# Performance work log

Measured on AMD Instinct MI355X. Metric: run time of the kernel, lower is better.

The kernel has to match this reference:

```python
import jax, jax.numpy as jnp
import numpy as np

DIM = 768
HEADS = 12
FF = 3072
EPS = 1e-6


def setup_inputs() -> dict:
    key = jax.random.key(0)
    ks = jax.random.split(key, 12)
    B, S, D, F_ = 64, 197, DIM, FF
    s = 0.02
    inp = {
        "x": jax.random.normal(ks[0], (B, S, D), jnp.float32),
        "Wq": jax.random.normal(ks[1], (D, D), jnp.float32) * s,
        "bq": jnp.zeros((D,), jnp.float32),
        "Wk": jax.random.normal(ks[2], (D, D), jnp.float32) * s,
        "bk": jnp.zeros((D,), jnp.float32),
        "Wv": jax.random.normal(ks[3], (D, D), jnp.float32) * s,
        "bv": jnp.zeros((D,), jnp.float32),
        "Wo": jax.random.normal(ks[4], (D, D), jnp.float32) * s,
        "bo": jnp.zeros((D,), jnp.float32),
        "ln1_w": jnp.ones((D,), jnp.float32),
        "ln1_b": jnp.zeros((D,), jnp.float32),
        "W1": jax.random.normal(ks[5], (D, F_), jnp.float32) * s,
        "b1": jnp.zeros((F_,), jnp.float32),
        "W2": jax.random.normal(ks[6], (F_, D), jnp.float32) * s,
        "b2": jnp.zeros((D,), jnp.float32),
        "ln2_w": jnp.ones((D,), jnp.float32),
        "ln2_b": jnp.zeros((D,), jnp.float32),
        "mask": jnp.ones((B, S), jnp.int32),
    }
    return inp


def _layernorm(x, w, b):
    m = jnp.mean(x, axis=-1, keepdims=True)
    v = jnp.mean(jnp.square(x - m), axis=-1, keepdims=True)  # unbiased=False
    return (x - m) / jnp.sqrt(v + EPS) * w + b


def _block(x, mask_f, Wq, bq, Wk, bk, Wv, bv, Wo, bo, ln1_w, ln1_b, W1, b1, W2, b2, ln2_w, ln2_b):
    B, S, D = x.shape
    H = HEADS
    Dh = D // H
    # --- attention (pre-norm) ---
    h = _layernorm(x, ln1_w, ln1_b)
    q = (h @ Wq + bq).reshape(B, S, H, Dh).transpose(0, 2, 1, 3)
    k = (h @ Wk + bk).reshape(B, S, H, Dh).transpose(0, 2, 1, 3)
    v = (h @ Wv + bv).reshape(B, S, H, Dh).transpose(0, 2, 1, 3)
    scores = jnp.einsum("bhqd,bhkd->bhqk", q, k) / jnp.sqrt(jnp.float32(Dh))
    scores = scores - 10000.0 * (1.0 - mask_f[:, None, None, :])
    probs = jax.nn.softmax(scores, axis=-1)
    attn = jnp.einsum("bhqk,bhkd->bhqd", probs, v).transpose(0, 2, 1, 3).reshape(B, S, D)
    x = x + (attn @ Wo + bo)  # dropout = identity (eval)
    # --- FFN (pre-norm), exact erf GELU (F.gelu default) ---
    h = _layernorm(x, ln2_w, ln2_b)
    h = jax.nn.gelu(h @ W1 + b1, approximate=False)
    x = x + (h @ W2 + b2)
    return x


def reference(x, Wq, bq, Wk, bk, Wv, bv, Wo, bo, ln1_w, ln1_b, W1, b1, W2, b2, ln2_w, ln2_b, mask):
    mask_f = mask.astype(jnp.float32)
    return _block(x, mask_f, Wq, bq, Wk, bk, Wv, bv, Wo, bo, ln1_w, ln1_b, W1, b1, W2, b2, ln2_w, ln2_b)
```

## Files before the change

kernel.cpp:

```cpp
#include <hip/hip_runtime.h>
#include <stdint.h>

#define B_   64
#define S_   197
#define D_   768
#define H_   12
#define F_   3072
#define BS_  (B_ * S_)

typedef __attribute__((ext_vector_type(8))) short short8;
typedef __attribute__((ext_vector_type(4))) float f32x4;

__device__ __forceinline__ float bf2f(unsigned short h) {
    union { unsigned int u; float f; } v; v.u = ((unsigned int)h) << 16; return v.f;
}
__device__ __forceinline__ unsigned short f2bf(float f) {
    union { float f; unsigned int u; } v; v.f = f;
    unsigned int r = v.u + 0x7FFFu + ((v.u >> 16) & 1u);
    return (unsigned short)(r >> 16);
}

__device__ __forceinline__ void g2l16(const void* g, void* l) {
    __builtin_amdgcn_global_load_lds(
        (const __attribute__((address_space(1))) unsigned int*)g,
        (__attribute__((address_space(3))) unsigned int*)l, 16, 0, 0);
}

__device__ __forceinline__ float gelu_f(float c) {
    float z = fabsf(c) * 0.70710678118f;
    float t = __builtin_amdgcn_rcpf(1.f + 0.3275911f * z);
    float p = ((((1.061405429f * t - 1.453152027f) * t + 1.421413741f) * t
               - 0.284496736f) * t + 0.254829592f) * t;
    float erfv = 1.f - p * __expf(-z * z);
    erfv = c < 0.f ? -erfv : erfv;
    return 0.5f * c * (1.f + erfv);
}

__global__ __launch_bounds__(256)
void transpose_all(const float* __restrict__ Wq, const float* __restrict__ Wk,
                   const float* __restrict__ Wv, const float* __restrict__ Wo,
                   const float* __restrict__ W1, const float* __restrict__ W2,
                   const float* __restrict__ bq, const float* __restrict__ bk,
                   const float* __restrict__ bv,
                   unsigned short* __restrict__ wqkvT, unsigned short* __restrict__ woT,
                   unsigned short* __restrict__ w1T, unsigned short* __restrict__ w2T,
                   float* __restrict__ bcat) {
    int blk = blockIdx.x;
    int tx = threadIdx.x, ty = threadIdx.y;
    if (blk == 6912) {
        for (int i = ty * 32 + tx; i < 2304; i += 256)
            bcat[i] = i < 768 ? bq[i] : (i < 1536 ? bk[i - 768] : bv[i - 1536]);
        return;
    }
    const float* W; unsigned short* Wt; int K, N, rel, nx;
    if (blk < 2304) {
        int m = blk / 576; rel = blk - m * 576; K = 768; N = 768; nx = 24;
        W  = m == 0 ? Wq : m == 1 ? Wk : m == 2 ? Wv : Wo;
        Wt = m < 3 ? wqkvT + (size_t)m * 768 * 768 : woT;
    } else if (blk < 4608) {
        rel = blk - 2304; K = 768; N = 3072; nx = 96; W = W1; Wt = w1T;
    } else {
        rel = blk - 4608; K = 3072; N = 768; nx = 24; W = W2; Wt = w2T;
    }
    int n0 = (rel % nx) * 32, k0 = (rel / nx) * 32;
    __shared__ float t[32][33];
#pragma unroll
    for (int i = ty; i < 32; i += 8) t[i][tx] = W[(size_t)(k0 + i) * N + n0 + tx];
    __syncthreads();
#pragma unroll
    for (int i = ty; i < 32; i += 8) Wt[(size_t)(n0 + i) * K + k0 + tx] = f2bf(t[tx][i]);
}

__global__ __launch_bounds__(256)
void ln_kernel(const float* __restrict__ x, const float* __restrict__ w,
               const float* __restrict__ b, unsigned short* __restrict__ out) {
    int row = blockIdx.x; size_t base = (size_t)row * 768;
    int tid = threadIdx.x;
    float v0 = x[base + tid], v1 = x[base + tid + 256], v2 = x[base + tid + 512];
    float s1 = v0 + v1 + v2;
    float s2 = v0 * v0 + v1 * v1 + v2 * v2;
#pragma unroll
    for (int off = 32; off > 0; off >>= 1) { s1 += __shfl_xor(s1, off); s2 += __shfl_xor(s2, off); }
    __shared__ float sa[4], sb[4];
    int w4 = tid >> 6;
    if ((tid & 63) == 0) { sa[w4] = s1; sb[w4] = s2; }
    __syncthreads();
    s1 = sa[0] + sa[1] + sa[2] + sa[3];
    s2 = sb[0] + sb[1] + sb[2] + sb[3];
    float mean = s1 * (1.f / 768.f);
    float var  = s2 * (1.f / 768.f) - mean * mean;
    float rstd = rsqrtf(var + 1e-6f);
    out[base + tid]       = f2bf((v0 - mean) * rstd * w[tid]       + b[tid]);
    out[base + tid + 256] = f2bf((v1 - mean) * rstd * w[tid + 256] + b[tid + 256]);
    out[base + tid + 512] = f2bf((v2 - mean) * rstd * w[tid + 512] + b[tid + 512]);
}

template<int MODE>
__global__ __launch_bounds__(64, 3)
void gemm1w(const unsigned short* __restrict__ A, const unsigned short* __restrict__ Bt,
            const float* __restrict__ bias, const float* __restrict__ resid,
            void* __restrict__ out, int M, int N, int K, int NSUP) {
    constexpr int BK = 32;
    __shared__ unsigned short As[2][64 * BK];
    __shared__ unsigned short Bs[2][64 * BK];
    const int l = threadIdx.x;
    const int lr = l & 15, lg = l >> 4;

    const int nN = gridDim.x, nM = gridDim.y;
    const int nTot = nN * nM;
    const int orig = blockIdx.x + nN * blockIdx.y;
    const int q8 = nTot >> 3, r8 = nTot & 7;
    const int xcd = orig & 7, idx = orig >> 3;
    const int rank = (xcd < r8 ? xcd * (q8 + 1) : r8 * (q8 + 1) + (xcd - r8) * q8) + idx;
    const int fullg = nM * NSUP;
    const int sup = rank / fullg;
    const int rem = rank - sup * fullg;
    const int n0s = sup * NSUP;
    int wsup = nN - n0s; if (wsup > NSUP) wsup = NSUP;
    const int mloc = rem / wsup;
    const int nloc = rem - mloc * wsup;
    const int bm0 = mloc * 64;
    const int bn0 = (n0s + nloc) * 64;

    const int srow = l >> 2;
    const int slb  = (l & 3) ^ ((l >> 3) & 3);
    const unsigned short* aBase = A  + (size_t)(bm0 + srow) * K + slb * 8;
    const unsigned short* bBase = Bt + (size_t)(bn0 + srow) * K + slb * 8;
    auto stage = [&](int buf, int kt) {
        const int k0 = kt * BK;
#pragma unroll
        for (int c = 0; c < 4; ++c) {
            g2l16(aBase + (size_t)c * 16 * K + k0, &As[buf][c * 16 * BK]);
            g2l16(bBase + (size_t)c * 16 * K + k0, &Bs[buf][c * 16 * BK]);
        }
    };

    f32x4 acc[4][4];
#pragma unroll
    for (int i = 0; i < 4; ++i)
#pragma unroll
        for (int j = 0; j < 4; ++j) acc[i][j] = (f32x4){0.f, 0.f, 0.f, 0.f};

    const int NK = K / BK;
    stage(0, 0);
    stage(1, 1);

    const int rblk = (lg ^ ((lr >> 1) & 3)) * 8;
    for (int kt = 0; kt < NK; ++kt) {
        const int buf = kt & 1;
        if (kt + 1 < NK) { asm volatile("s_waitcnt vmcnt(8)" ::: "memory"); }
        else             { asm volatile("s_waitcnt vmcnt(0)" ::: "memory"); }
        __builtin_amdgcn_sched_barrier(0);
        short8 af[4], bfr[4];
#pragma unroll
        for (int mt = 0; mt < 4; ++mt) af[mt]  = *(const short8*)&As[buf][(mt * 16 + lr) * BK + rblk];
#pragma unroll
        for (int nt = 0; nt < 4; ++nt) bfr[nt] = *(const short8*)&Bs[buf][(nt * 16 + lr) * BK + rblk];
        __builtin_amdgcn_sched_barrier(0);
        if (kt + 2 < NK) stage(buf, kt + 2);
#pragma unroll
        for (int mt = 0; mt < 4; ++mt)
#pragma unroll
            for (int nt = 0; nt < 4; ++nt)
                acc[mt][nt] = __builtin_amdgcn_mfma_f32_16x16x32_bf16(af[mt], bfr[nt], acc[mt][nt], 0, 0, 0);
    }

#pragma unroll
    for (int mt = 0; mt < 4; ++mt)
#pragma unroll
        for (int nt = 0; nt < 4; ++nt)
#pragma unroll
            for (int r = 0; r < 4; ++r) {
                int gm = bm0 + mt * 16 + lg * 4 + r;
                int gn = bn0 + nt * 16 + lr;
                float c = acc[mt][nt][r] + bias[gn];
                if (MODE == 0) {
                    if (gn < 768) c *= 0.125f;
                    ((unsigned short*)out)[(size_t)gm * N + gn] = f2bf(c);
                } else if (MODE == 1) {
                    ((float*)out)[(size_t)gm * N + gn] = c + resid[(size_t)gm * N + gn];
                } else {
                    ((unsigned short*)out)[(size_t)gm * N + gn] = f2bf(gelu_f(c));
                }
            }
}

__global__ __launch_bounds__(256)
void attn_mfma(const unsigned short* __restrict__ qkv, const int* __restrict__ mask,
               unsigned short* __restrict__ ctx) {
    __shared__ unsigned short Ks[208 * 64];
    __shared__ unsigned short Vt[64 * 256];
    __shared__ unsigned short Psl[4][16 * 40];
    __shared__ float maskadj[224];
    const int bh = blockIdx.x, b = bh / 12, h = bh - b * 12;
    const int tid = threadIdx.x, l = tid & 63, w = tid >> 6;
    const int lr = l & 15, lg = l >> 4;
    const unsigned short* Qg = qkv + (size_t)b * 197 * 2304 + h * 64;
    const unsigned short* Kg = Qg + 768;
    const unsigned short* Vg = Qg + 1536;

    if (tid < 224)
        maskadj[tid] = tid < 197 ? -10000.f * (1.f - (float)mask[b * 197 + tid]) : -1e30f;

    for (int c = w; c < 26; c += 4) {
        int row = c * 8 + (l >> 3);
        int rc = row < 197 ? row : 196;
        int blk = (l & 7) ^ (row & 7);
        g2l16(Kg + (size_t)rc * 2304 + blk * 8, &Ks[c * 8 * 64]);
    }
    {
        int jj = tid >> 3, db = tid & 7;
#pragma unroll
        for (int it = 0; it < 7; ++it) {
            int j = it * 32 + jj;
            short8 v = (short8){0, 0, 0, 0, 0, 0, 0, 0};
            if (j < 197) v = *(const short8*)(Vg + (size_t)j * 2304 + db * 8);
#pragma unroll
            for (int e = 0; e < 8; ++e) {
                int d = db * 8 + e;
                Vt[d * 256 + (((j >> 3) ^ (d & 7)) * 8) + (j & 7)] = (unsigned short)v[e];
            }
        }
    }
    __syncthreads();

    for (int t = w; t < 13; t += 4) {
        const int q0 = t * 16;
        int qr = q0 + lr; qr = qr < 197 ? qr : 196;
        const short8 qf0 = *(const short8*)(Qg + (size_t)qr * 2304 + lg * 8);
        const short8 qf1 = *(const short8*)(Qg + (size_t)qr * 2304 + 32 + lg * 8);

        f32x4 sc[13];
#pragma unroll
        for (int kt = 0; kt < 13; ++kt) {
            const int krow = kt * 16 + lr;
            const short8 kf0 = *(const short8*)&Ks[krow * 64 + ((lg ^ (lr & 7)) * 8)];
            const short8 kf1 = *(const short8*)&Ks[krow * 64 + (((4 + lg) ^ (lr & 7)) * 8)];
            f32x4 a = (f32x4){0.f, 0.f, 0.f, 0.f};
            a = __builtin_amdgcn_mfma_f32_16x16x32_bf16(qf0, kf0, a, 0, 0, 0);
            a = __builtin_amdgcn_mfma_f32_16x16x32_bf16(qf1, kf1, a, 0, 0, 0);
            sc[kt] = a;
        }
        float mx[4] = {-1e30f, -1e30f, -1e30f, -1e30f};
#pragma unroll
        for (int kt = 0; kt < 13; ++kt) {
            float ma = maskadj[kt * 16 + lr];
#pragma unroll
            for (int r = 0; r < 4; ++r) {
                sc[kt][r] += ma;
                mx[r] = fmaxf(mx[r], sc[kt][r]);
            }
        }
#pragma unroll
        for (int r = 0; r < 4; ++r) {
            mx[r] = fmaxf(mx[r], __shfl_xor(mx[r], 1));
            mx[r] = fmaxf(mx[r], __shfl_xor(mx[r], 2));
            mx[r] = fmaxf(mx[r], __shfl_xor(mx[r], 4));
            mx[r] = fmaxf(mx[r], __shfl_xor(mx[r], 8));
        }
        float sm[4] = {0.f, 0.f, 0.f, 0.f};
#pragma unroll
        for (int kt = 0; kt < 13; ++kt)
#pragma unroll
            for (int r = 0; r < 4; ++r) {
                float p = __expf(sc[kt][r] - mx[r]);
                sc[kt][r] = p;
                sm[r] += p;
            }
#pragma unroll
        for (int r = 0; r < 4; ++r) {
            sm[r] += __shfl_xor(sm[r], 1);
            sm[r] += __shfl_xor(sm[r], 2);
            sm[r] += __shfl_xor(sm[r], 4);
            sm[r] += __shfl_xor(sm[r], 8);
            sm[r] = 1.f / sm[r];
        }
        f32x4 ao[4];
#pragma unroll
        for (int dt = 0; dt < 4; ++dt) ao[dt] = (f32x4){0.f, 0.f, 0.f, 0.f};
        unsigned short* Pw = &Psl[w][0];
#pragma unroll
        for (int ks = 0; ks < 7; ++ks) {
#pragma unroll
            for (int tl = 0; tl < 2; ++tl) {
                const int kt = ks * 2 + tl;
#pragma unroll
                for (int r = 0; r < 4; ++r) {
                    unsigned short pv = 0;
                    if (kt < 13) pv = f2bf(sc[kt][r] * sm[r]);
                    Pw[(lg * 4 + r) * 40 + tl * 16 + lr] = pv;
                }
            }
            const short8 pf = *(const short8*)&Pw[lr * 40 + lg * 8];
#pragma unroll
            for (int dt = 0; dt < 4; ++dt) {
                const int drow = dt * 16 + lr;
                const short8 vf = *(const short8*)&Vt[drow * 256 + (((4 * ks + lg) ^ (lr & 7)) * 8)];
                ao[dt] = __builtin_amdgcn_mfma_f32_16x16x32_bf16(vf, pf, ao[dt], 0, 0, 0);
            }
        }
        const int q = q0 + lr;
        if (q < 197) {
            unsigned short* crow = ctx + ((size_t)b * 197 + q) * 768 + h * 64;
#pragma unroll
            for (int dt = 0; dt < 4; ++dt) {
                union { unsigned short u[4]; uint2 v; } pk;
#pragma unroll
                for (int r = 0; r < 4; ++r) pk.u[r] = f2bf(ao[dt][r]);
                *(uint2*)(crow + dt * 16 + lg * 4) = pk.v;
            }
        }
    }
}

extern "C" void kernel_launch(void* const* d_in, const int* in_sizes, int n_in,
                              void* d_out, int out_size, void* d_ws, size_t ws_size,
                              hipStream_t stream) {
    const float* x    = (const float*)d_in[0];
    const float* Wq   = (const float*)d_in[1];
    const float* bq   = (const float*)d_in[2];
    const float* Wk   = (const float*)d_in[3];
    const float* bk   = (const float*)d_in[4];
    const float* Wv   = (const float*)d_in[5];
    const float* bv   = (const float*)d_in[6];
    const float* Wo   = (const float*)d_in[7];
    const float* bo   = (const float*)d_in[8];
    const float* ln1w = (const float*)d_in[9];
    const float* ln1b = (const float*)d_in[10];
    const float* W1   = (const float*)d_in[11];
    const float* b1   = (const float*)d_in[12];
    const float* W2   = (const float*)d_in[13];
    const float* b2   = (const float*)d_in[14];
    const float* ln2w = (const float*)d_in[15];
    const float* ln2b = (const float*)d_in[16];
    const int*   mask = (const int*)d_in[17];

    size_t off = 0;
    auto nxt = [&](size_t bytes) -> void* {
        void* r = (char*)d_ws + off; off += (bytes + 255) & ~(size_t)255; return r;
    };
    unsigned short* hbuf  = (unsigned short*)nxt((size_t)BS_ * 768 * 2);
    unsigned short* qkvg  = (unsigned short*)nxt((size_t)BS_ * 3072 * 2);
    unsigned short* wqkvT = (unsigned short*)nxt((size_t)2304 * 768 * 2);
    unsigned short* woT   = (unsigned short*)nxt((size_t)768 * 768 * 2);
    unsigned short* w1T   = (unsigned short*)nxt((size_t)3072 * 768 * 2);
    unsigned short* w2T   = (unsigned short*)nxt((size_t)768 * 3072 * 2);
    float*          bcat  = (float*)nxt(2304 * 4);
    unsigned short* ctx   = (unsigned short*)nxt((size_t)BS_ * 768 * 2);
    (void)ws_size; (void)in_sizes; (void)n_in; (void)out_size;

    transpose_all<<<6913, dim3(32, 8), 0, stream>>>(Wq, Wk, Wv, Wo, W1, W2, bq, bk, bv,
                                                    wqkvT, woT, w1T, w2T, bcat);
    ln_kernel<<<BS_, 256, 0, stream>>>(x, ln1w, ln1b, hbuf);
    gemm1w<0><<<dim3(36, 197), 64, 0, stream>>>(hbuf, wqkvT, bcat, nullptr, qkvg, BS_, 2304, 768, 18);
    attn_mfma<<<768, 256, 0, stream>>>(qkvg, mask, ctx);
    gemm1w<1><<<dim3(12, 197), 64, 0, stream>>>(ctx, woT, bo, x, d_out, BS_, 768, 768, 12);
    ln_kernel<<<BS_, 256, 0, stream>>>((const float*)d_out, ln2w, ln2b, hbuf);
    gemm1w<2><<<dim3(48, 197), 64, 0, stream>>>(hbuf, w1T, b1, nullptr, qkvg, BS_, 3072, 768, 24);
    gemm1w<1><<<dim3(12, 197), 64, 0, stream>>>(qkvg, w2T, b2, (const float*)d_out, d_out, BS_, 768, 3072, 6);
}
```

Measured before the change: 490.6 us.

## Replace single-wave 64x64 GEMM with 8-wave 256x256 tiled pipelined GEMM

Replaces the 64-thread 64x64-tile GEMM with a 512-thread kernel that computes 256x256 output tiles. Each of its 8 waves owns a 128x64 sub-tile, BK is 64, LDS reads use an XOR swizzle, and the next K-tile's global-to-LDS loads are interleaved between MFMA phases using barriers and setprio. The larger tiles raise data reuse per LDS byte and cut global traffic. The cost is bounds clamping for the M tail (12608 is not a multiple of 256), fewer blocks (450 for the QKV GEMM, 150 for the projection GEMMs), and 128 KB of LDS per block.

```diff
diff --git a/kernel.cpp b/kernel.cpp
--- a/kernel.cpp
+++ b/kernel.cpp
@@ -96,15 +96,16 @@
 }
 
 template<int MODE>
-__global__ __launch_bounds__(64, 3)
-void gemm1w(const unsigned short* __restrict__ A, const unsigned short* __restrict__ Bt,
-            const float* __restrict__ bias, const float* __restrict__ resid,
-            void* __restrict__ out, int M, int N, int K, int NSUP) {
-    constexpr int BK = 32;
-    __shared__ unsigned short As[2][64 * BK];
-    __shared__ unsigned short Bs[2][64 * BK];
-    const int l = threadIdx.x;
+__global__ __launch_bounds__(512)
+void gemmT(const unsigned short* __restrict__ A, const unsigned short* __restrict__ Bt,
+           const float* __restrict__ bias, const float* __restrict__ resid,
+           void* __restrict__ out, int M, int N, int K, int NSUP) {
+    __shared__ unsigned short As[2][256 * 64];
+    __shared__ unsigned short Bs[2][256 * 64];
+    const int tid = threadIdx.x;
+    const int l = tid & 63, wid = tid >> 6;
     const int lr = l & 15, lg = l >> 4;
+    const int wr = wid >> 2, wc = wid & 3;
 
     const int nN = gridDim.x, nM = gridDim.y;
     const int nTot = nN * nM;
@@ -119,68 +120,121 @@
     int wsup = nN - n0s; if (wsup > NSUP) wsup = NSUP;
     const int mloc = rem / wsup;
     const int nloc = rem - mloc * wsup;
-    const int bm0 = mloc * 64;
-    const int bn0 = (n0s + nloc) * 64;
-
-    const int srow = l >> 2;
-    const int slb  = (l & 3) ^ ((l >> 3) & 3);
-    const unsigned short* aBase = A  + (size_t)(bm0 + srow) * K + slb * 8;
-    const unsigned short* bBase = Bt + (size_t)(bn0 + srow) * K + slb * 8;
-    auto stage = [&](int buf, int kt) {
-        const int k0 = kt * BK;
-#pragma unroll
-        for (int c = 0; c < 4; ++c) {
-            g2l16(aBase + (size_t)c * 16 * K + k0, &As[buf][c * 16 * BK]);
-            g2l16(bBase + (size_t)c * 16 * K + k0, &Bs[buf][c * 16 * BK]);
-        }
+    const int bm0 = mloc * 256;
+    const int bn0 = (n0s + nloc) * 256;
+
+    const int sr = wid * 8 + (l >> 3);
+    const int slb = (l & 7) ^ (l >> 3);
+    auto stA = [&](int kt, int qr) {
+        int gr = bm0 + qr * 64 + sr; gr = gr < M ? gr : M - 1;
+        g2l16(A + (size_t)gr * K + kt * 64 + slb * 8, &As[kt & 1][(qr * 64 + wid * 8) * 64]);
     };
-
-    f32x4 acc[4][4];
-#pragma unroll
-    for (int i = 0; i < 4; ++i)
+    auto stB = [&](int kt, int qr) {
+        int gr = bn0 + qr * 64 + sr;
+        g2l16(Bt + (size_t)gr * K + kt * 64 + slb * 8, &Bs[kt & 1][(qr * 64 + wid * 8) * 64]);
+    };
+
+    f32x4 acc[8][4];
+#pragma unroll
+    for (int i = 0; i < 8; ++i)
 #pragma unroll
         for (int j = 0; j < 4; ++j) acc[i][j] = (f32x4){0.f, 0.f, 0.f, 0.f};
 
-    const int NK = K / BK;
-    stage(0, 0);
-    stage(1, 1);
-
-    const int rblk = (lg ^ ((lr >> 1) & 3)) * 8;
-    for (int kt = 0; kt < NK; ++kt) {
+    const int NKT = K >> 6;
+#pragma unroll
+    for (int qr = 0; qr < 4; ++qr) stA(0, qr);
+#pragma unroll
+    for (int qr = 0; qr < 4; ++qr) stB(0, qr);
+#pragma unroll
+    for (int qr = 0; qr < 4; ++qr) stA(1, qr);
+#pragma unroll
+    for (int qr = 0; qr < 4; ++qr) stB(1, qr);
+
+    const int rx = lr & 7;
+    for (int kt = 0; kt < NKT; ++kt) {
         const int buf = kt & 1;
-        if (kt + 1 < NK) { asm volatile("s_waitcnt vmcnt(8)" ::: "memory"); }
-        else             { asm volatile("s_waitcnt vmcnt(0)" ::: "memory"); }
+        const bool mid = (kt >= 1) && (kt + 1 < NKT);
+        const bool st2 = (kt + 2 < NKT);
+        const unsigned short* Ab = &As[buf][0];
+        const unsigned short* Bb = &Bs[buf][0];
+        short8 af[4][2], bf[2][2];
+
+        auto rdA = [&](int mh) {
+#pragma unroll
+            for (int mt = 0; mt < 4; ++mt)
+#pragma unroll
+                for (int kk = 0; kk < 2; ++kk)
+                    af[mt][kk] = *(const short8*)&Ab[(wr * 128 + mh * 64 + mt * 16 + lr) * 64 +
+                                                     (((kk * 4 + lg) ^ rx) * 8)];
+        };
+        auto rdB = [&](int nh) {
+#pragma unroll
+            for (int nt = 0; nt < 2; ++nt)
+#pragma unroll
+                for (int kk = 0; kk < 2; ++kk)
+                    bf[nt][kk] = *(const short8*)&Bb[(wc * 64 + nh * 32 + nt * 16 + lr) * 64 +
+                                                     (((kk * 4 + lg) ^ rx) * 8)];
+        };
+        auto mfma16 = [&](int mh, int nh) {
+            __builtin_amdgcn_s_barrier();
+            asm volatile("s_waitcnt lgkmcnt(0)" ::: "memory");
+            __builtin_amdgcn_sched_barrier(0);
+            __builtin_amdgcn_s_setprio(1);
+#pragma unroll
+            for (int mt = 0; mt < 4; ++mt)
+#pragma unroll
+                for (int nt = 0; nt < 2; ++nt)
+#pragma unroll
+                    for (int kk = 0; kk < 2; ++kk)
+                        acc[mh * 4 + mt][nh * 2 + nt] = __builtin_amdgcn_mfma_f32_16x16x32_bf16(
+                            af[mt][kk], bf[nt][kk], acc[mh * 4 + mt][nh * 2 + nt], 0, 0, 0);
+            __builtin_amdgcn_s_setprio(0);
+        };
+
+        if (kt == 0)       { asm volatile("s_waitcnt vmcnt(8)" ::: "memory"); }
+        else if (st2)      { asm volatile("s_waitcnt vmcnt(1)" ::: "memory"); }
+        else               { asm volatile("s_waitcnt vmcnt(0)" ::: "memory"); }
+        __builtin_amdgcn_s_barrier();
         __builtin_amdgcn_sched_barrier(0);
-        short8 af[4], bfr[4];
-#pragma unroll
-        for (int mt = 0; mt < 4; ++mt) af[mt]  = *(const short8*)&As[buf][(mt * 16 + lr) * BK + rblk];
-#pragma unroll
-        for (int nt = 0; nt < 4; ++nt) bfr[nt] = *(const short8*)&Bs[buf][(nt * 16 + lr) * BK + rblk];
+        rdA(0); rdB(0);
+        if (mid) { stB(kt + 1, 0); stA(kt + 1, 1); }
+        mfma16(0, 0);
+        rdB(1);
+        if (mid) { stB(kt + 1, 1); stA(kt + 1, 3); }
+        mfma16(0, 1);
+        if (kt == 1)       { asm volatile("s_waitcnt vmcnt(6)" ::: "memory"); }
+        else if (st2)      { asm volatile("s_waitcnt vmcnt(8)" ::: "memory"); }
+        else               { asm volatile("s_waitcnt vmcnt(0)" ::: "memory"); }
+        __builtin_amdgcn_s_barrier();
         __builtin_amdgcn_sched_barrier(0);
-        if (kt + 2 < NK) stage(buf, kt + 2);
-#pragma unroll
-        for (int mt = 0; mt < 4; ++mt)
-#pragma unroll
-            for (int nt = 0; nt < 4; ++nt)
-                acc[mt][nt] = __builtin_amdgcn_mfma_f32_16x16x32_bf16(af[mt], bfr[nt], acc[mt][nt], 0, 0, 0);
-    }
-
-#pragma unroll
-    for (int mt = 0; mt < 4; ++mt)
+        rdA(1); rdB(0);
+        if (mid) stB(kt + 1, 2);
+        if (st2) stA(kt + 2, 0);
+        mfma16(1, 0);
+        rdB(1);
+        if (mid) stB(kt + 1, 3);
+        if (st2) stA(kt + 2, 2);
+        mfma16(1, 1);
+    }
+
+#pragma unroll
+    for (int mt = 0; mt < 8; ++mt)
 #pragma unroll
         for (int nt = 0; nt < 4; ++nt)
 #pragma unroll
             for (int r = 0; r < 4; ++r) {
-                int gm = bm0 + mt * 16 + lg * 4 + r;
-                int gn = bn0 + nt * 16 + lr;
-                float c = acc[mt][nt][r] + bias[gn];
-                if (MODE == 0) {
-                    if (gn < 768) c *= 0.125f;
-                    ((unsigned short*)out)[(size_t)gm * N + gn] = f2bf(c);
-                } else if (MODE == 1) {
-                    ((float*)out)[(size_t)gm * N + gn] = c + resid[(size_t)gm * N + gn];
-                } else {
-                    ((unsigned short*)out)[(size_t)gm * N + gn] = f2bf(gelu_f(c));
+                int gm = bm0 + wr * 128 + mt * 16 + lg * 4 + r;
+                int gn = bn0 + wc * 64 + nt * 16 + lr;
+                if (gm < M) {
+                    float c = acc[mt][nt][r] + bias[gn];
+                    if (MODE == 0) {
+                        if (gn < 768) c *= 0.125f;
+                        ((unsigned short*)out)[(size_t)gm * N + gn] = f2bf(c);
+                    } else if (MODE == 1) {
+                        ((float*)out)[(size_t)gm * N + gn] = c + resid[(size_t)gm * N + gn];
+                    } else {
+                        ((unsigned short*)out)[(size_t)gm * N + gn] = f2bf(gelu_f(c));
+                    }
                 }
             }
 }
@@ -352,10 +406,10 @@
     transpose_all<<<6913, dim3(32, 8), 0, stream>>>(Wq, Wk, Wv, Wo, W1, W2, bq, bk, bv,
                                                     wqkvT, woT, w1T, w2T, bcat);
     ln_kernel<<<BS_, 256, 0, stream>>>(x, ln1w, ln1b, hbuf);
-    gemm1w<0><<<dim3(36, 197), 64, 0, stream>>>(hbuf, wqkvT, bcat, nullptr, qkvg, BS_, 2304, 768, 18);
+    gemmT<0><<<dim3(9, 50), 512, 0, stream>>>(hbuf, wqkvT, bcat, nullptr, qkvg, BS_, 2304, 768, 5);
     attn_mfma<<<768, 256, 0, stream>>>(qkvg, mask, ctx);
-    gemm1w<1><<<dim3(12, 197), 64, 0, stream>>>(ctx, woT, bo, x, d_out, BS_, 768, 768, 12);
+    gemmT<1><<<dim3(3, 50), 512, 0, stream>>>(ctx, woT, bo, x, d_out, BS_, 768, 768, 3);
     ln_kernel<<<BS_, 256, 0, stream>>>((const float*)d_out, ln2w, ln2b, hbuf);
-    gemm1w<2><<<dim3(48, 197), 64, 0, stream>>>(hbuf, w1T, b1, nullptr, qkvg, BS_, 3072, 768, 24);
-    gemm1w<1><<<dim3(12, 197), 64, 0, stream>>>(qkvg, w2T, b2, (const float*)d_out, d_out, BS_, 768, 3072, 6);
-}
+    gemmT<2><<<dim3(12, 50), 512, 0, stream>>>(hbuf, w1T, b1, nullptr, qkvg, BS_, 3072, 768, 6);
+    gemmT<1><<<dim3(3, 50), 512, 0, stream>>>(qkvg, w2T, b2, (const float*)d_out, d_out, BS_, 768, 3072, 3);
+}
```

Measured after the change: 479.8 us. 2.2% less time.
